# Optimization experiments

Hardware: AMD Instinct MI355X
Metric: run time of the kernel (lower is better)

Reference implementation:

```python
import jax, jax.numpy as jnp
import numpy as np
from jax import lax

B, S, I, H = 32, 2048, 256, 512


def setup_inputs() -> dict:
    key = jax.random.key(0)
    ks = jax.random.split(key, 6)
    stdv = 1.0 / np.sqrt(H)
    return {
        "inputs": jax.random.normal(ks[0], (B, S, I), dtype=jnp.float32),
        "h0": jax.random.normal(ks[1], (1, B, H), dtype=jnp.float32),
        "weight_ih": jax.random.uniform(ks[2], (H, I), minval=-stdv, maxval=stdv, dtype=jnp.float32),
        "weight_hh": jax.random.uniform(ks[3], (H, H), minval=-stdv, maxval=stdv, dtype=jnp.float32),
        "bias_ih": jax.random.uniform(ks[4], (H,), minval=-stdv, maxval=stdv, dtype=jnp.float32),
        "bias_hh": jax.random.uniform(ks[5], (H,), minval=-stdv, maxval=stdv, dtype=jnp.float32),
    }


def reference(inputs, h0, weight_ih, weight_hh, bias_ih, bias_hh):
    # Precompute input projections for all timesteps: [B, S, H]
    z_in = jnp.einsum("bsi,hi->bsh", inputs, weight_ih) + bias_ih

    def step(h_prev, z_t):
        # h_t = relu(z_t + h_{t-1} @ W_hh^T + b_hh)
        h = jax.nn.relu(z_t + h_prev @ weight_hh.T + bias_hh)
        return h, h

    h_final, outs = lax.scan(step, h0[0], jnp.swapaxes(z_in, 0, 1))  # scan over time
    output = jnp.swapaxes(outs, 0, 1)  # [B, S, H]
    return output, h_final[None]  # ([B,S,H], [1,B,H])
```

## Files before the change

kernel.cpp:

```cpp
#include <hip/hip_runtime.h>

#define B_SZ 32
#define S_LEN 2048
#define I_SZ 256
#define H_SZ 512
#define OUT_MAIN ((size_t)B_SZ * S_LEN * H_SZ)

#define KT_TOT 16
#define KT_REG 12
#define KT_LDS 4

typedef _Float16 half8 __attribute__((ext_vector_type(8)));
typedef float floatx4 __attribute__((ext_vector_type(4)));
typedef unsigned long long u64;

#define LDS_BARRIER()                                         \
  do {                                                        \
    __builtin_amdgcn_sched_barrier(0);                        \
    asm volatile("s_waitcnt lgkmcnt(0)" ::: "memory");        \
    __builtin_amdgcn_s_barrier();                             \
    __builtin_amdgcn_sched_barrier(0);                        \
  } while (0)

__global__ void rnn_init(const float* __restrict__ wih, const float* __restrict__ whh,
                         const float* __restrict__ h0,
                         _Float16* __restrict__ wih16, _Float16* __restrict__ w2,
                         _Float16* __restrict__ h16) {
  int idx = blockIdx.x * blockDim.x + threadIdx.x;
  int stride = gridDim.x * blockDim.x;
  for (int i = idx; i < H_SZ * I_SZ; i += stride) wih16[i] = (_Float16)wih[i];
  for (int o = idx; o < H_SZ * H_SZ; o += stride) {
    const int e = o & 7;
    const int lane = (o >> 3) & 63;
    const int mt = (o >> 9) & 31;
    const int kt = o >> 14;
    const int m = mt * 16 + (lane & 15);
    const int k = kt * 32 + (lane >> 4) * 8 + e;
    w2[o] = (_Float16)whh[(size_t)m * H_SZ + k];
  }
  for (int i = idx; i < B_SZ * H_SZ; i += stride) h16[i] = (_Float16)h0[i];
}

__launch_bounds__(256, 2)
__global__ void rnn_zin(const float* __restrict__ inputs, const _Float16* __restrict__ wih16,
                        const float* __restrict__ bih, const float* __restrict__ bhh,
                        float* __restrict__ out) {
  const int wave = threadIdx.x >> 6;
  const int lane = threadIdx.x & 63;
  const int col = lane & 15;
  const int quad = lane >> 4;
  const int m0 = blockIdx.x * 64 + wave * 16;

  floatx4 acc[32];
#pragma unroll
  for (int nt = 0; nt < 32; ++nt) acc[nt] = (floatx4){0.f, 0.f, 0.f, 0.f};

#pragma unroll
  for (int kt = 0; kt < 8; ++kt) {
    const float* ap = inputs + (size_t)(m0 + col) * I_SZ + kt * 32 + quad * 8;
    float4 a0 = *(const float4*)(ap);
    float4 a1 = *(const float4*)(ap + 4);
    half8 af;
    af[0] = (_Float16)a0.x; af[1] = (_Float16)a0.y; af[2] = (_Float16)a0.z; af[3] = (_Float16)a0.w;
    af[4] = (_Float16)a1.x; af[5] = (_Float16)a1.y; af[6] = (_Float16)a1.z; af[7] = (_Float16)a1.w;
#pragma unroll
    for (int nt = 0; nt < 32; ++nt) {
      half8 bf = *(const half8*)(wih16 + (size_t)(nt * 16 + col) * I_SZ + kt * 32 + quad * 8);
      acc[nt] = __builtin_amdgcn_mfma_f32_16x16x32_f16(af, bf, acc[nt], 0, 0, 0);
    }
  }

#pragma unroll
  for (int nt = 0; nt < 32; ++nt) {
    const int j = nt * 16 + col;
    const float bias = bih[j] + bhh[j];
#pragma unroll
    for (int r = 0; r < 4; ++r) {
      const int m = m0 + quad * 4 + r;
      out[(size_t)m * H_SZ + j] = acc[nt][r] + bias;
    }
  }
}

__launch_bounds__(256, 1)
__global__ void rnn_steps(const _Float16* __restrict__ w2, float* __restrict__ out,
                          const _Float16* __restrict__ h16) {
  __shared__ _Float16 lds_w[KT_LDS * 32 * 64 * 8];
  __shared__ _Float16 lds_h[16 * H_SZ];

  const int tid = threadIdx.x;
  const int w = tid >> 6;
  const int lane = tid & 63;
  const int col = lane & 15;
  const int quad = lane >> 4;
  const int gb = blockIdx.x;
  const int b = gb * 16 + col;

  {
    const uint4* src = (const uint4*)(w2 + (size_t)KT_REG * 32 * 64 * 8);
    uint4* dst = (uint4*)lds_w;
    for (int i = tid; i < (KT_LDS * 32 * 64 * 8) / 8; i += 256) dst[i] = src[i];
  }
  for (int g = tid; g < 16 * (H_SZ / 4); g += 256) {
    const int c = g >> 7;
    const int j = (g & 127) * 4;
    u64 v = *(const u64*)(h16 + (size_t)(gb * 16 + c) * H_SZ + j);
    *(u64*)((char*)lds_h + c * 1024 + ((j * 2) ^ ((c & 7) << 4))) = v;
  }

  half8 wReg[8][KT_REG];
#pragma unroll
  for (int mt = 0; mt < 8; ++mt)
#pragma unroll
    for (int kt = 0; kt < KT_REG; ++kt)
      wReg[mt][kt] = *(const half8*)(w2 + ((size_t)(kt * 32 + w * 8 + mt) * 64 + lane) * 8);

  __syncthreads();

#pragma unroll 1
  for (int t = 0; t < S_LEN; ++t) {
    float4 zf[8];
#pragma unroll
    for (int mt = 0; mt < 8; ++mt) {
      const int j = w * 128 + mt * 16 + quad * 4;
      zf[mt] = *(const float4*)(out + ((size_t)b * S_LEN + t) * H_SZ + j);
    }

    floatx4 acc[8];
#pragma unroll
    for (int mt = 0; mt < 8; ++mt) acc[mt] = (floatx4){0.f, 0.f, 0.f, 0.f};

#pragma unroll
    for (int kt = 0; kt < KT_TOT; ++kt) {
      const half8 hf = *(const half8*)((const char*)lds_h + col * 1024 +
                                       ((kt * 64 + quad * 16) ^ ((col & 7) << 4)));
      if (kt < KT_REG) {
#pragma unroll
        for (int mt = 0; mt < 8; ++mt)
          acc[mt] = __builtin_amdgcn_mfma_f32_16x16x32_f16(wReg[mt][kt], hf, acc[mt], 0, 0, 0);
      } else {
#pragma unroll
        for (int mt = 0; mt < 8; ++mt) {
          const half8 wl = *(const half8*)((const char*)lds_w +
              ((size_t)((kt - KT_REG) * 32 + w * 8 + mt) * 64 + lane) * 16);
          acc[mt] = __builtin_amdgcn_mfma_f32_16x16x32_f16(wl, hf, acc[mt], 0, 0, 0);
        }
      }
    }

    LDS_BARRIER();

#pragma unroll
    for (int mt = 0; mt < 8; ++mt) {
      const int j = w * 128 + mt * 16 + quad * 4;
      float4 hv;
      hv.x = fmaxf(zf[mt].x + acc[mt][0], 0.f);
      hv.y = fmaxf(zf[mt].y + acc[mt][1], 0.f);
      hv.z = fmaxf(zf[mt].z + acc[mt][2], 0.f);
      hv.w = fmaxf(zf[mt].w + acc[mt][3], 0.f);
      *(float4*)(out + ((size_t)b * S_LEN + t) * H_SZ + j) = hv;
      union { _Float16 h[4]; u64 q; } pk;
      pk.h[0] = (_Float16)hv.x; pk.h[1] = (_Float16)hv.y;
      pk.h[2] = (_Float16)hv.z; pk.h[3] = (_Float16)hv.w;
      *(u64*)((char*)lds_h + col * 1024 + ((j * 2) ^ ((col & 7) << 4))) = pk.q;
      if (t == S_LEN - 1)
        *(float4*)(out + OUT_MAIN + (size_t)b * H_SZ + j) = hv;
    }

    LDS_BARRIER();
  }
}

extern "C" void kernel_launch(void* const* d_in, const int* in_sizes, int n_in,
                              void* d_out, int out_size, void* d_ws, size_t ws_size,
                              hipStream_t stream) {
  (void)in_sizes; (void)n_in; (void)out_size; (void)ws_size;
  const float* inputs = (const float*)d_in[0];
  const float* h0     = (const float*)d_in[1];
  const float* wih    = (const float*)d_in[2];
  const float* whh    = (const float*)d_in[3];
  const float* bih    = (const float*)d_in[4];
  const float* bhh    = (const float*)d_in[5];
  float* out = (float*)d_out;

  char* ws = (char*)d_ws;
  _Float16* wih16 = (_Float16*)(ws);
  _Float16* w2    = (_Float16*)(ws + 262144);
  _Float16* h16   = (_Float16*)(ws + 262144 + 524288);

  rnn_init<<<64, 256, 0, stream>>>(wih, whh, h0, wih16, w2, h16);
  rnn_zin<<<1024, 256, 0, stream>>>(inputs, wih16, bih, bhh, out);
  rnn_steps<<<2, 256, 0, stream>>>(w2, out, h16);
}
```

Before: 6.939 ms.

## Store hidden state in MFMA fragment layout and software-pipeline LDS reads

The hidden state in LDS is rearranged into the MFMA B-fragment layout, so each lane reads its fragment with a linear lane*16 address and no XOR swizzle. The h0 initialisation in rnn_init writes the same fragment layout. The step loop double-buffers the h-fragment reads in groups of four k-tiles so LDS loads overlap the MFMAs. The ReLU is computed before the barrier, and the global output store moves after the second barrier, off the critical LDS write path. Risks are extra register pressure from the hA/hB buffers and possible LDS bank conflicts in the new write pattern.

```diff
diff --git a/kernel.cpp b/kernel.cpp
--- a/kernel.cpp
+++ b/kernel.cpp
@@ -25,7 +25,7 @@
 __global__ void rnn_init(const float* __restrict__ wih, const float* __restrict__ whh,
                          const float* __restrict__ h0,
                          _Float16* __restrict__ wih16, _Float16* __restrict__ w2,
-                         _Float16* __restrict__ h16) {
+                         _Float16* __restrict__ h16f) {
   int idx = blockIdx.x * blockDim.x + threadIdx.x;
   int stride = gridDim.x * blockDim.x;
   for (int i = idx; i < H_SZ * I_SZ; i += stride) wih16[i] = (_Float16)wih[i];
@@ -38,7 +38,15 @@
     const int k = kt * 32 + (lane >> 4) * 8 + e;
     w2[o] = (_Float16)whh[(size_t)m * H_SZ + k];
   }
-  for (int i = idx; i < B_SZ * H_SZ; i += stride) h16[i] = (_Float16)h0[i];
+  for (int i = idx; i < 2 * 16 * 64 * 8; i += stride) {
+    const int e = i & 7;
+    const int l = (i >> 3) & 63;
+    const int kt = (i >> 9) & 15;
+    const int g = i >> 13;
+    const int b = g * 16 + (l & 15);
+    const int k = kt * 32 + ((l >> 4) & 3) * 8 + e;
+    h16f[i] = (_Float16)h0[(size_t)b * H_SZ + k];
+  }
 }
 
 __launch_bounds__(256, 2)
@@ -84,9 +92,9 @@
 
 __launch_bounds__(256, 1)
 __global__ void rnn_steps(const _Float16* __restrict__ w2, float* __restrict__ out,
-                          const _Float16* __restrict__ h16) {
+                          const _Float16* __restrict__ h16f) {
   __shared__ _Float16 lds_w[KT_LDS * 32 * 64 * 8];
-  __shared__ _Float16 lds_h[16 * H_SZ];
+  __shared__ _Float16 lds_h[16 * 64 * 8];
 
   const int tid = threadIdx.x;
   const int w = tid >> 6;
@@ -95,80 +103,116 @@
   const int quad = lane >> 4;
   const int gb = blockIdx.x;
   const int b = gb * 16 + col;
+  const int w8 = w * 8;
+
+  const char* lds_hc = (const char*)lds_h;
+  const char* lds_wc = (const char*)lds_w;
+  const int lane16 = lane * 16;
 
   {
     const uint4* src = (const uint4*)(w2 + (size_t)KT_REG * 32 * 64 * 8);
     uint4* dst = (uint4*)lds_w;
     for (int i = tid; i < (KT_LDS * 32 * 64 * 8) / 8; i += 256) dst[i] = src[i];
   }
-  for (int g = tid; g < 16 * (H_SZ / 4); g += 256) {
-    const int c = g >> 7;
-    const int j = (g & 127) * 4;
-    u64 v = *(const u64*)(h16 + (size_t)(gb * 16 + c) * H_SZ + j);
-    *(u64*)((char*)lds_h + c * 1024 + ((j * 2) ^ ((c & 7) << 4))) = v;
+  {
+    const u64* src = (const u64*)(h16f + (size_t)gb * 8192);
+    u64* dst = (u64*)lds_h;
+    for (int i = tid; i < 2048; i += 256) dst[i] = src[i];
   }
 
   half8 wReg[8][KT_REG];
 #pragma unroll
-  for (int mt = 0; mt < 8; ++mt)
+  for (int mm = 0; mm < 8; ++mm)
 #pragma unroll
     for (int kt = 0; kt < KT_REG; ++kt)
-      wReg[mt][kt] = *(const half8*)(w2 + ((size_t)(kt * 32 + w * 8 + mt) * 64 + lane) * 8);
+      wReg[mm][kt] = *(const half8*)(w2 + ((size_t)(kt * 32 + w8 + mm) * 64 + lane) * 8);
 
   __syncthreads();
+
+  const float* zbase = out + (size_t)b * S_LEN * H_SZ + w * 128 + quad * 4;
+  char* hw = (char*)lds_h + w * 4096 + (quad >> 1) * 256 + col * 16 + (quad & 1) * 8;
+
+#define HRD(kt) (*(const half8*)(lds_hc + (kt)*1024 + lane16))
+#define WRD(kt, mm) (*(const half8*)(lds_wc + ((size_t)(((kt)-12) * 32 + w8 + (mm))) * 1024 + lane16))
 
 #pragma unroll 1
   for (int t = 0; t < S_LEN; ++t) {
+    floatx4 acc[8];
+#pragma unroll
+    for (int mm = 0; mm < 8; ++mm) acc[mm] = (floatx4){0.f, 0.f, 0.f, 0.f};
+
+    half8 hA[4], hB[4];
+#pragma unroll
+    for (int q = 0; q < 4; ++q) hA[q] = HRD(q);
+
     float4 zf[8];
 #pragma unroll
-    for (int mt = 0; mt < 8; ++mt) {
-      const int j = w * 128 + mt * 16 + quad * 4;
-      zf[mt] = *(const float4*)(out + ((size_t)b * S_LEN + t) * H_SZ + j);
-    }
-
-    floatx4 acc[8];
-#pragma unroll
-    for (int mt = 0; mt < 8; ++mt) acc[mt] = (floatx4){0.f, 0.f, 0.f, 0.f};
-
-#pragma unroll
-    for (int kt = 0; kt < KT_TOT; ++kt) {
-      const half8 hf = *(const half8*)((const char*)lds_h + col * 1024 +
-                                       ((kt * 64 + quad * 16) ^ ((col & 7) << 4)));
-      if (kt < KT_REG) {
-#pragma unroll
-        for (int mt = 0; mt < 8; ++mt)
-          acc[mt] = __builtin_amdgcn_mfma_f32_16x16x32_f16(wReg[mt][kt], hf, acc[mt], 0, 0, 0);
-      } else {
-#pragma unroll
-        for (int mt = 0; mt < 8; ++mt) {
-          const half8 wl = *(const half8*)((const char*)lds_w +
-              ((size_t)((kt - KT_REG) * 32 + w * 8 + mt) * 64 + lane) * 16);
-          acc[mt] = __builtin_amdgcn_mfma_f32_16x16x32_f16(wl, hf, acc[mt], 0, 0, 0);
-        }
-      }
+    for (int mm = 0; mm < 8; ++mm) zf[mm] = *(const float4*)(zbase + (size_t)t * H_SZ + mm * 16);
+
+#pragma unroll
+    for (int q = 0; q < 4; ++q) hB[q] = HRD(4 + q);
+#pragma unroll
+    for (int q = 0; q < 4; ++q)
+#pragma unroll
+      for (int mm = 0; mm < 8; ++mm)
+        acc[mm] = __builtin_amdgcn_mfma_f32_16x16x32_f16(wReg[mm][q], hA[q], acc[mm], 0, 0, 0);
+
+#pragma unroll
+    for (int q = 0; q < 4; ++q) hA[q] = HRD(8 + q);
+#pragma unroll
+    for (int q = 0; q < 4; ++q)
+#pragma unroll
+      for (int mm = 0; mm < 8; ++mm)
+        acc[mm] = __builtin_amdgcn_mfma_f32_16x16x32_f16(wReg[mm][4 + q], hB[q], acc[mm], 0, 0, 0);
+
+#pragma unroll
+    for (int q = 0; q < 4; ++q) hB[q] = HRD(12 + q);
+#pragma unroll
+    for (int q = 0; q < 4; ++q)
+#pragma unroll
+      for (int mm = 0; mm < 8; ++mm)
+        acc[mm] = __builtin_amdgcn_mfma_f32_16x16x32_f16(wReg[mm][8 + q], hA[q], acc[mm], 0, 0, 0);
+
+#pragma unroll
+    for (int kt = 12; kt < 16; ++kt) {
+      half8 wl[8];
+#pragma unroll
+      for (int mm = 0; mm < 8; ++mm) wl[mm] = WRD(kt, mm);
+#pragma unroll
+      for (int mm = 0; mm < 8; ++mm)
+        acc[mm] = __builtin_amdgcn_mfma_f32_16x16x32_f16(wl[mm], hB[kt - 12], acc[mm], 0, 0, 0);
+    }
+
+    float4 hv[8];
+#pragma unroll
+    for (int mm = 0; mm < 8; ++mm) {
+      hv[mm].x = fmaxf(zf[mm].x + acc[mm][0], 0.f);
+      hv[mm].y = fmaxf(zf[mm].y + acc[mm][1], 0.f);
+      hv[mm].z = fmaxf(zf[mm].z + acc[mm][2], 0.f);
+      hv[mm].w = fmaxf(zf[mm].w + acc[mm][3], 0.f);
     }
 
     LDS_BARRIER();
 
 #pragma unroll
-    for (int mt = 0; mt < 8; ++mt) {
-      const int j = w * 128 + mt * 16 + quad * 4;
-      float4 hv;
-      hv.x = fmaxf(zf[mt].x + acc[mt][0], 0.f);
-      hv.y = fmaxf(zf[mt].y + acc[mt][1], 0.f);
-      hv.z = fmaxf(zf[mt].z + acc[mt][2], 0.f);
-      hv.w = fmaxf(zf[mt].w + acc[mt][3], 0.f);
-      *(float4*)(out + ((size_t)b * S_LEN + t) * H_SZ + j) = hv;
+    for (int mm = 0; mm < 8; ++mm) {
       union { _Float16 h[4]; u64 q; } pk;
-      pk.h[0] = (_Float16)hv.x; pk.h[1] = (_Float16)hv.y;
-      pk.h[2] = (_Float16)hv.z; pk.h[3] = (_Float16)hv.w;
-      *(u64*)((char*)lds_h + col * 1024 + ((j * 2) ^ ((col & 7) << 4))) = pk.q;
+      pk.h[0] = (_Float16)hv[mm].x; pk.h[1] = (_Float16)hv[mm].y;
+      pk.h[2] = (_Float16)hv[mm].z; pk.h[3] = (_Float16)hv[mm].w;
+      *(u64*)(hw + ((mm >> 1) * 1024 + (mm & 1) * 512)) = pk.q;
+    }
+
+    LDS_BARRIER();
+
+#pragma unroll
+    for (int mm = 0; mm < 8; ++mm) {
+      *(float4*)(const_cast<float*>(zbase) + (size_t)t * H_SZ + mm * 16) = hv[mm];
       if (t == S_LEN - 1)
-        *(float4*)(out + OUT_MAIN + (size_t)b * H_SZ + j) = hv;
-    }
-
-    LDS_BARRIER();
-  }
+        *(float4*)(out + OUT_MAIN + (size_t)b * H_SZ + w * 128 + mm * 16 + quad * 4) = hv[mm];
+    }
+  }
+#undef HRD
+#undef WRD
 }
 
 extern "C" void kernel_launch(void* const* d_in, const int* in_sizes, int n_in,
@@ -186,9 +230,9 @@
   char* ws = (char*)d_ws;
   _Float16* wih16 = (_Float16*)(ws);
   _Float16* w2    = (_Float16*)(ws + 262144);
-  _Float16* h16   = (_Float16*)(ws + 262144 + 524288);
-
-  rnn_init<<<64, 256, 0, stream>>>(wih, whh, h0, wih16, w2, h16);
+  _Float16* h16f  = (_Float16*)(ws + 262144 + 524288);
+
+  rnn_init<<<64, 256, 0, stream>>>(wih, whh, h0, wih16, w2, h16f);
   rnn_zin<<<1024, 256, 0, stream>>>(inputs, wih16, bih, bhh, out);
-  rnn_steps<<<2, 256, 0, stream>>>(w2, out, h16);
-}
+  rnn_steps<<<2, 256, 0, stream>>>(w2, out, h16f);
+}
```

New measurement: 7.788 ms. +12.2%, slower.
